# Kernel tuning notes

Hardware: AMD Instinct MI355X
Metric: run time of the kernel (lower is better)

Reference implementation:

```python
import jax, jax.numpy as jnp
import numpy as np

EPS = 1e-5
GROUPS = 32


def group_norm(x, gamma, beta):
    b, c, h, w = x.shape
    xg = x.reshape(b, GROUPS, c // GROUPS, h, w)
    mu = xg.mean(axis=(2, 3, 4), keepdims=True)
    var = xg.var(axis=(2, 3, 4), keepdims=True)
    xn = ((xg - mu) * jax.lax.rsqrt(var + EPS)).reshape(b, c, h, w)
    return xn * gamma[None, :, None, None] + beta[None, :, None, None]


def setup_inputs() -> dict:
    key = jax.random.key(0)
    ks = jax.random.split(key, 4)
    b, c, h, w = 4, 512, 64, 64
    x = jax.random.normal(ks[0], (b, c, h, w), dtype=jnp.float32)
    gn_w = jnp.ones((c,), jnp.float32)
    gn_b = jnp.zeros((c,), jnp.float32)
    qkv_w = jax.random.normal(ks[1], (3 * c, c), dtype=jnp.float32) * (c ** -0.5)
    qkv_b = jnp.zeros((3 * c,), jnp.float32)
    out_w = jax.random.normal(ks[2], (c, c), dtype=jnp.float32) * (c ** -0.5)
    out_b = jnp.zeros((c,), jnp.float32)
    return {"x": x, "gn_w": gn_w, "gn_b": gn_b, "qkv_w": qkv_w,
            "qkv_b": qkv_b, "out_w": out_w, "out_b": out_b}


def reference(x, gn_w, gn_b, qkv_w, qkv_b, out_w, out_b):
    b, c, hh, ww = x.shape
    n = hh * ww
    h = group_norm(x, gn_w, gn_b)
    # 1x1 conv == per-pixel matmul over channels
    qkv = jnp.einsum('bchw,oc->bohw', h, qkv_w) + qkv_b[None, :, None, None]
    q, k, v = jnp.split(qkv, 3, axis=1)
    q = q.transpose(0, 2, 3, 1).reshape(b, n, c)   # (b, n, c)
    k = k.reshape(b, c, n)                          # (b, c, n)
    v = v.transpose(0, 2, 3, 1).reshape(b, n, c)   # (b, n, c)
    attn = jax.nn.softmax(jnp.einsum('bnc,bcm->bnm', q, k) * (c ** -0.5), axis=-1)
    out = jnp.einsum('bnm,bmc->bnc', attn, v)
    out = out.reshape(b, hh, ww, c).transpose(0, 3, 1, 2)
    out = jnp.einsum('bchw,oc->bohw', out, out_w) + out_b[None, :, None, None]
    return out + x
```

## Files before the change

### kernel.cpp

```cpp
#include <hip/hip_runtime.h>
#include <cmath>

#define NB 4
#define NC 512
#define NN 4096
#define ATTN_SCALE 0.04419417382415922f

typedef __bf16 bf16x8 __attribute__((ext_vector_type(8)));
typedef float floatx4 __attribute__((ext_vector_type(4)));

__device__ __forceinline__ unsigned short f2bf(float f) {
    union { float f; unsigned int u; } v; v.f = f;
    return (unsigned short)((v.u + 0x7fffu + ((v.u >> 16) & 1u)) >> 16);
}
__device__ __forceinline__ unsigned short f2bf_trunc(float f) {
    union { float f; unsigned int u; } v; v.f = f;
    return (unsigned short)(v.u >> 16);
}
__device__ __forceinline__ float bf2f(unsigned short u) {
    union { unsigned int u; float f; } v; v.u = ((unsigned int)u) << 16;
    return v.f;
}

__device__ __forceinline__ void gload_lds16(const unsigned short* gp, unsigned short* lp) {
    __builtin_amdgcn_global_load_lds(
        (const __attribute__((address_space(1))) void*)gp,
        (__attribute__((address_space(3))) void*)lp, 16, 0, 0);
}

__global__ __launch_bounds__(256) void gn_partial_kernel(
    const float* __restrict__ x, float* __restrict__ part)
{
    int blk = blockIdx.x;
    int bg = blk >> 3, sub = blk & 7;
    const float4* xv = (const float4*)(x + (size_t)bg * 16 * NN + (size_t)sub * 8192);
    float s1 = 0.f, s2 = 0.f;
#pragma unroll
    for (int i = 0; i < 8; ++i) {
        float4 v = xv[threadIdx.x + i * 256];
        s1 += v.x + v.y + v.z + v.w;
        s2 += v.x * v.x + v.y * v.y + v.z * v.z + v.w * v.w;
    }
#pragma unroll
    for (int off = 32; off; off >>= 1) {
        s1 += __shfl_xor(s1, off, 64);
        s2 += __shfl_xor(s2, off, 64);
    }
    __shared__ float r1[4], r2[4];
    int lane = threadIdx.x & 63, w = threadIdx.x >> 6;
    if (lane == 0) { r1[w] = s1; r2[w] = s2; }
    __syncthreads();
    if (threadIdx.x == 0) {
        part[blk * 2]     = r1[0] + r1[1] + r1[2] + r1[3];
        part[blk * 2 + 1] = r2[0] + r2[1] + r2[2] + r2[3];
    }
}

__global__ __launch_bounds__(128) void gn_final_kernel(
    const float* __restrict__ part, const float* __restrict__ gw,
    const float* __restrict__ gb, float* __restrict__ ss)
{
    int tg = threadIdx.x;
    int b = tg >> 5, g = tg & 31;
    float s1 = 0.f, s2 = 0.f;
#pragma unroll
    for (int s = 0; s < 8; ++s) {
        s1 += part[(tg * 8 + s) * 2];
        s2 += part[(tg * 8 + s) * 2 + 1];
    }
    float mean = s1 * (1.0f / 65536.0f);
    float var  = s2 * (1.0f / 65536.0f) - mean * mean;
    float rstd = rsqrtf(var + 1e-5f);
#pragma unroll
    for (int i = 0; i < 16; ++i) {
        int c = g * 16 + i;
        float sc = rstd * gw[c];
        ss[b * NC + c] = sc;
        ss[2048 + b * NC + c] = gb[c] - mean * sc;
    }
}

__global__ __launch_bounds__(256) void wconv_kernel(
    const float* __restrict__ qkv_w, const float* __restrict__ out_w,
    unsigned short* __restrict__ wq, unsigned short* __restrict__ wo)
{
    int i = blockIdx.x * 256 + threadIdx.x;
    const int NQ = 1536 * 512;
    if (i < NQ) wq[i] = f2bf(qkv_w[i]);
    else        wo[i - NQ] = f2bf(out_w[i - NQ]);
}

__global__ __launch_bounds__(256) void htnorm_kernel(
    const float* __restrict__ x, const float* __restrict__ ss,
    unsigned short* __restrict__ ht)
{
    int b = blockIdx.z;
    int c0 = blockIdx.y * 32, n0 = blockIdx.x * 32;
    __shared__ float T[32][33];
    int tx = threadIdx.x & 31, ty = threadIdx.x >> 5;
    const float* xb = x + ((size_t)b * NC + c0) * NN;
    const float* sc = ss + b * NC + c0;
    const float* sh = ss + 2048 + b * NC + c0;
#pragma unroll
    for (int i = 0; i < 4; ++i) {
        int c = ty + i * 8;
        T[c][tx] = xb[(size_t)c * NN + n0 + tx] * sc[c] + sh[c];
    }
    __syncthreads();
    unsigned short* hb = ht + ((size_t)b * NN + n0) * NC + c0;
#pragma unroll
    for (int i = 0; i < 4; ++i) {
        int n = ty + i * 8;
        hb[(size_t)n * NC + tx] = f2bf(T[tx][n]);
    }
}

template<int MODE, int BM, int BN>
__global__ __launch_bounds__(256, 3) void mfma_gemm(
    const unsigned short* __restrict__ Abase,
    const unsigned short* __restrict__ Bbase,
    const float* __restrict__ e0, const float* __restrict__ e1,
    float* __restrict__ outf,
    unsigned short* __restrict__ ob0, unsigned short* __restrict__ ob1)
{
    constexpr int K = 512;
    constexpr int FI = BM / 32;
    constexpr int FJ = BN / 32;
    const int z = blockIdx.z;
    const size_t bnc = (size_t)NN * NC;
    const size_t bss = (size_t)NN * NN;

    const unsigned short* A;
    const unsigned short* B;
    if constexpr (MODE == 0)      { A = Abase + (size_t)z * bnc; B = Bbase; }
    else if constexpr (MODE == 1) { A = Abase; B = Bbase + (size_t)z * bnc; }
    else if constexpr (MODE == 2) { A = Abase + (size_t)z * bnc; B = Bbase + (size_t)z * bnc; }
    else                          { A = Abase; B = Bbase + (size_t)z * bnc; }

    const int m0 = blockIdx.y * BM;
    const int n0 = blockIdx.x * BN;

    __shared__ __attribute__((aligned(16))) unsigned short As[BM * 32];
    __shared__ __attribute__((aligned(16))) unsigned short Bs[BN * 32];

    const int t = threadIdx.x;
    const int lane = t & 63;
    const int w = t >> 6;
    const int wr = w >> 1, wc = w & 1;

    const int sr = w * 16 + (lane >> 2);
    const int sc8 = (lane & 3) * 8;
    const int lds_elem = w * 512;

    floatx4 acc[FI][FJ] = {};

    for (int k0 = 0; k0 < K; k0 += 32) {
#pragma unroll
        for (int s = 0; s < BM / 64; ++s)
            gload_lds16(A + (size_t)(m0 + s * 64 + sr) * K + k0 + sc8,
                        As + s * 2048 + lds_elem);
#pragma unroll
        for (int s = 0; s < BN / 64; ++s)
            gload_lds16(B + (size_t)(n0 + s * 64 + sr) * K + k0 + sc8,
                        Bs + s * 2048 + lds_elem);
        __syncthreads();

        bf16x8 af[FI], bfr[FJ];
        const unsigned short* Ab = As + ((wr * (BM / 2) + (lane & 15)) * 32) + (lane >> 4) * 8;
        const unsigned short* Bb = Bs + ((wc * (BN / 2) + (lane & 15)) * 32) + (lane >> 4) * 8;
#pragma unroll
        for (int i = 0; i < FI; ++i) af[i]  = *(const bf16x8*)(Ab + i * 16 * 32);
#pragma unroll
        for (int j = 0; j < FJ; ++j) bfr[j] = *(const bf16x8*)(Bb + j * 16 * 32);
#pragma unroll
        for (int i = 0; i < FI; ++i)
#pragma unroll
            for (int j = 0; j < FJ; ++j)
                acc[i][j] = __builtin_amdgcn_mfma_f32_16x16x32_bf16(
                    af[i], bfr[j], acc[i][j], 0, 0, 0);
        __syncthreads();
    }

    const int fr = lane >> 4;
    const int fc = lane & 15;

    if constexpr (MODE == 2) {
        float rs[FI][4];
#pragma unroll
        for (int i = 0; i < FI; ++i)
#pragma unroll
            for (int r = 0; r < 4; ++r) rs[i][r] = 0.f;
#pragma unroll
        for (int i = 0; i < FI; ++i) {
#pragma unroll
            for (int j = 0; j < FJ; ++j) {
                int n = n0 + wc * (BN / 2) + j * 16 + fc;
                int mbase = m0 + wr * (BM / 2) + i * 16 + fr * 4;
#pragma unroll
                for (int r = 0; r < 4; ++r) {
                    float e = __expf(acc[i][j][r]);
                    ob0[(size_t)z * bss + (size_t)(mbase + r) * NN + n] = f2bf_trunc(e);
                    rs[i][r] += e;
                }
            }
        }
#pragma unroll
        for (int i = 0; i < FI; ++i) {
#pragma unroll
            for (int r = 0; r < 4; ++r) {
                float v = rs[i][r];
                v += __shfl_xor(v, 1, 16);
                v += __shfl_xor(v, 2, 16);
                v += __shfl_xor(v, 4, 16);
                v += __shfl_xor(v, 8, 16);
                if (fc == 0) {
                    int m = m0 + wr * (BM / 2) + i * 16 + fr * 4 + r;
                    atomicAdd(&outf[z * NN + m], v);
                }
            }
        }
        return;
    }

#pragma unroll
    for (int i = 0; i < FI; ++i) {
#pragma unroll
        for (int j = 0; j < FJ; ++j) {
            int n = n0 + wc * (BN / 2) + j * 16 + fc;
            int mbase = m0 + wr * (BM / 2) + i * 16 + fr * 4;
#pragma unroll
            for (int r = 0; r < 4; ++r) {
                int m = mbase + r;
                float val = acc[i][j][r];
                if constexpr (MODE == 0) {
                    val += e0[n];
                    if (n < 512) ob0[((size_t)z * NN + m) * NC + n] = f2bf(val * ATTN_SCALE);
                    else         ob1[((size_t)z * NN + m) * NC + (n - 512)] = f2bf(val);
                } else if constexpr (MODE == 1) {
                    val += e0[1024 + m];
                    ob0[((size_t)z * NC + m) * NN + n] = f2bf(val);
                } else {
                    size_t idx = ((size_t)z * NC + m) * NN + n;
                    outf[idx] = val + e0[m] + e1[idx];
                }
            }
        }
    }
}

__global__ __launch_bounds__(256, 4) void pv_gemm(
    const unsigned short* __restrict__ Abase,
    const unsigned short* __restrict__ Bbase,
    const float* __restrict__ L,
    unsigned short* __restrict__ Ob)
{
    const int id = blockIdx.x;
    const int xcd = id & 7;
    const int j0 = id >> 3;
    const int ct = j0 & 3;
    const int pairl = j0 >> 2;
    const int p = pairl * 8 + xcd;
    const int ptile = p & 63, z = p >> 6;

    const size_t bss = (size_t)NN * NN, bnc = (size_t)NN * NC;
    const unsigned short* A = Abase + (size_t)z * bss;
    const unsigned short* B = Bbase + (size_t)z * bnc;
    const int m0 = ptile * 64;
    const int n0 = ct * 128;

    __shared__ __attribute__((aligned(16))) unsigned short As[64 * 64];
    __shared__ __attribute__((aligned(16))) unsigned short Bs[128 * 64];

    const int t = threadIdx.x;
    const int lane = t & 63;
    const int w = t >> 6;
    const int wr = w >> 1, wc = w & 1;

    const int sr = w * 8 + (lane >> 3);
    const int scs = ((lane & 7) ^ (lane >> 3)) * 8;
    const int lds_elem = w * 512;

    floatx4 acc[2][4] = {};

    for (int k0 = 0; k0 < NN; k0 += 64) {
#pragma unroll
        for (int s = 0; s < 2; ++s)
            gload_lds16(A + (size_t)(m0 + s * 32 + sr) * NN + k0 + scs,
                        As + s * 2048 + lds_elem);
#pragma unroll
        for (int s = 0; s < 4; ++s)
            gload_lds16(B + (size_t)(n0 + s * 32 + sr) * NN + k0 + scs,
                        Bs + s * 2048 + lds_elem);
        __syncthreads();

        bf16x8 af[2][2], bfr[4][2];
#pragma unroll
        for (int i = 0; i < 2; ++i) {
            const int ra = wr * 32 + i * 16 + (lane & 15);
#pragma unroll
            for (int kk = 0; kk < 2; ++kk)
                af[i][kk] = *(const bf16x8*)(As + ra * 64 +
                    (((kk * 4 + (lane >> 4)) ^ (ra & 7)) * 8));
        }
#pragma unroll
        for (int jj = 0; jj < 4; ++jj) {
            const int rb = wc * 64 + jj * 16 + (lane & 15);
#pragma unroll
            for (int kk = 0; kk < 2; ++kk)
                bfr[jj][kk] = *(const bf16x8*)(Bs + rb * 64 +
                    (((kk * 4 + (lane >> 4)) ^ (rb & 7)) * 8));
        }
#pragma unroll
        for (int kk = 0; kk < 2; ++kk)
#pragma unroll
            for (int i = 0; i < 2; ++i)
#pragma unroll
                for (int jj = 0; jj < 4; ++jj)
                    acc[i][jj] = __builtin_amdgcn_mfma_f32_16x16x32_bf16(
                        af[i][kk], bfr[jj][kk], acc[i][jj], 0, 0, 0);
        __syncthreads();
    }

    const int fr = lane >> 4;
    const int fc = lane & 15;
#pragma unroll
    for (int i = 0; i < 2; ++i) {
#pragma unroll
        for (int r = 0; r < 4; ++r) {
            int m = m0 + wr * 32 + i * 16 + fr * 4 + r;
            float linv = 1.0f / L[z * NN + m];
#pragma unroll
            for (int jj = 0; jj < 4; ++jj) {
                int n = n0 + wc * 64 + jj * 16 + fc;
                Ob[(size_t)z * bnc + (size_t)m * NC + n] = f2bf(acc[i][jj][r] * linv);
            }
        }
    }
}

extern "C" void kernel_launch(void* const* d_in, const int* in_sizes, int n_in,
                              void* d_out, int out_size, void* d_ws, size_t ws_size,
                              hipStream_t stream)
{
    const float* x     = (const float*)d_in[0];
    const float* gn_w  = (const float*)d_in[1];
    const float* gn_b  = (const float*)d_in[2];
    const float* qkv_w = (const float*)d_in[3];
    const float* qkv_b = (const float*)d_in[4];
    const float* out_w = (const float*)d_in[5];
    const float* out_b = (const float*)d_in[6];
    float* out = (float*)d_out;

    const size_t bnc = (size_t)NN * NC;
    char* w = (char*)d_ws;
    float* ss   = (float*)w;                 w += 16384;
    float* part = (float*)w;                 w += 8192;
    float* Lsum = (float*)w;                 w += (size_t)NB * NN * 4;
    unsigned short* wq = (unsigned short*)w; w += (size_t)1536 * 512 * 2;
    unsigned short* wo = (unsigned short*)w; w += (size_t)512 * 512 * 2;
    unsigned short* qt = (unsigned short*)w; w += NB * bnc * 2;
    unsigned short* kt = (unsigned short*)w; w += NB * bnc * 2;
    unsigned short* vt = (unsigned short*)w; w += NB * bnc * 2;
    unsigned short* SP = (unsigned short*)w; w += (size_t)NB * NN * NN * 2;
    unsigned short* ht = SP;
    unsigned short* Ob = qt;

    hipMemsetAsync(Lsum, 0, (size_t)NB * NN * sizeof(float), stream);

    gn_partial_kernel<<<1024, 256, 0, stream>>>(x, part);
    gn_final_kernel<<<1, 128, 0, stream>>>(part, gn_w, gn_b, ss);
    wconv_kernel<<<(1536 * 512 + 512 * 512) / 256, 256, 0, stream>>>(qkv_w, out_w, wq, wo);
    htnorm_kernel<<<dim3(NN / 32, NC / 32, NB), 256, 0, stream>>>(x, ss, ht);

    mfma_gemm<0, 128, 128><<<dim3(1024 / 128, NN / 128, NB), 256, 0, stream>>>(
        ht, wq, qkv_b, nullptr, nullptr, qt, kt);
    mfma_gemm<1, 128, 128><<<dim3(NN / 128, 512 / 128, NB), 256, 0, stream>>>(
        wq + (size_t)1024 * 512, ht, qkv_b, nullptr, nullptr, vt, nullptr);

    mfma_gemm<2, 128, 128><<<dim3(NN / 128, NN / 128, NB), 256, 0, stream>>>(
        qt, kt, nullptr, nullptr, Lsum, SP, nullptr);
    pv_gemm<<<dim3(1024), 256, 0, stream>>>(SP, vt, Lsum, Ob);

    mfma_gemm<4, 128, 128><<<dim3(NN / 128, 512 / 128, NB), 256, 0, stream>>>(
        wo, Ob, out_b, x, out, nullptr, nullptr);
}
```

Before: 378.2 us.

## Double-buffer LDS in MFMA GEMM, swizzle LDS layout, retile skinny GEMMs

Makes the GEMM's shared-memory staging double-buffered, so the global-to-LDS loads for the next K slice are issued before the MFMAs on the current slice run. It also applies an XOR swizzle to the K-slot column of the LDS tiles to cut bank conflicts on the fragment reads. The V projection and output projection GEMMs switch to 64x128 tiles with a higher minimum-blocks launch bound, giving more blocks on those small grids. In exchange the kernel uses twice the LDS, and the explicit vmcnt waits may limit how much load latency is actually hidden.

Measured after the change: 377.6 us. Within noise of the previous version (-0.1%).

```diff
diff --git a/kernel.cpp b/kernel.cpp
--- a/kernel.cpp
+++ b/kernel.cpp
@@ -115,8 +115,8 @@
     }
 }
 
-template<int MODE, int BM, int BN>
-__global__ __launch_bounds__(256, 3) void mfma_gemm(
+template<int MODE, int BM, int BN, int MINB>
+__global__ __launch_bounds__(256, MINB) void mfma_gemm(
     const unsigned short* __restrict__ Abase,
     const unsigned short* __restrict__ Bbase,
     const float* __restrict__ e0, const float* __restrict__ e1,
@@ -124,6 +124,7 @@
     unsigned short* __restrict__ ob0, unsigned short* __restrict__ ob1)
 {
     constexpr int K = 512;
+    constexpr int NT = K / 32;
     constexpr int FI = BM / 32;
     constexpr int FJ = BN / 32;
     const int z = blockIdx.z;
@@ -140,8 +141,8 @@
     const int m0 = blockIdx.y * BM;
     const int n0 = blockIdx.x * BN;
 
-    __shared__ __attribute__((aligned(16))) unsigned short As[BM * 32];
-    __shared__ __attribute__((aligned(16))) unsigned short Bs[BN * 32];
+    __shared__ __attribute__((aligned(16))) unsigned short As[2][BM * 32];
+    __shared__ __attribute__((aligned(16))) unsigned short Bs[2][BN * 32];
 
     const int t = threadIdx.x;
     const int lane = t & 63;
@@ -149,37 +150,55 @@
     const int wr = w >> 1, wc = w & 1;
 
     const int sr = w * 16 + (lane >> 2);
-    const int sc8 = (lane & 3) * 8;
+    const int scs = ((lane & 3) ^ ((lane >> 3) & 3)) * 8;
     const int lds_elem = w * 512;
+    const int kslot = lane >> 4;
 
     floatx4 acc[FI][FJ] = {};
 
-    for (int k0 = 0; k0 < K; k0 += 32) {
+    auto stage = [&](int buf, int k0) {
 #pragma unroll
         for (int s = 0; s < BM / 64; ++s)
-            gload_lds16(A + (size_t)(m0 + s * 64 + sr) * K + k0 + sc8,
-                        As + s * 2048 + lds_elem);
+            gload_lds16(A + (size_t)(m0 + s * 64 + sr) * K + k0 + scs,
+                        &As[buf][s * 2048 + lds_elem]);
 #pragma unroll
         for (int s = 0; s < BN / 64; ++s)
-            gload_lds16(B + (size_t)(n0 + s * 64 + sr) * K + k0 + sc8,
-                        Bs + s * 2048 + lds_elem);
-        __syncthreads();
-
+            gload_lds16(B + (size_t)(n0 + s * 64 + sr) * K + k0 + scs,
+                        &Bs[buf][s * 2048 + lds_elem]);
+    };
+
+    auto compute = [&](int buf) {
         bf16x8 af[FI], bfr[FJ];
-        const unsigned short* Ab = As + ((wr * (BM / 2) + (lane & 15)) * 32) + (lane >> 4) * 8;
-        const unsigned short* Bb = Bs + ((wc * (BN / 2) + (lane & 15)) * 32) + (lane >> 4) * 8;
-#pragma unroll
-        for (int i = 0; i < FI; ++i) af[i]  = *(const bf16x8*)(Ab + i * 16 * 32);
-#pragma unroll
-        for (int j = 0; j < FJ; ++j) bfr[j] = *(const bf16x8*)(Bb + j * 16 * 32);
+#pragma unroll
+        for (int i = 0; i < FI; ++i) {
+            const int ra = wr * (BM / 2) + i * 16 + (lane & 15);
+            af[i] = *(const bf16x8*)(&As[buf][ra * 32 + ((kslot ^ ((ra >> 1) & 3)) * 8)]);
+        }
+#pragma unroll
+        for (int j = 0; j < FJ; ++j) {
+            const int rb = wc * (BN / 2) + j * 16 + (lane & 15);
+            bfr[j] = *(const bf16x8*)(&Bs[buf][rb * 32 + ((kslot ^ ((rb >> 1) & 3)) * 8)]);
+        }
 #pragma unroll
         for (int i = 0; i < FI; ++i)
 #pragma unroll
             for (int j = 0; j < FJ; ++j)
                 acc[i][j] = __builtin_amdgcn_mfma_f32_16x16x32_bf16(
                     af[i], bfr[j], acc[i][j], 0, 0, 0);
+    };
+
+    stage(0, 0);
+    asm volatile("s_waitcnt vmcnt(0)" ::: "memory");
+    __syncthreads();
+    int cur = 0;
+    for (int kt = 0; kt < NT - 1; ++kt) {
+        stage(cur ^ 1, (kt + 1) * 32);
+        compute(cur);
+        asm volatile("s_waitcnt vmcnt(0)" ::: "memory");
         __syncthreads();
-    }
+        cur ^= 1;
+    }
+    compute(cur);
 
     const int fr = lane >> 4;
     const int fc = lane & 15;
@@ -372,15 +391,15 @@
     wconv_kernel<<<(1536 * 512 + 512 * 512) / 256, 256, 0, stream>>>(qkv_w, out_w, wq, wo);
     htnorm_kernel<<<dim3(NN / 32, NC / 32, NB), 256, 0, stream>>>(x, ss, ht);
 
-    mfma_gemm<0, 128, 128><<<dim3(1024 / 128, NN / 128, NB), 256, 0, stream>>>(
+    mfma_gemm<0, 128, 128, 3><<<dim3(1024 / 128, NN / 128, NB), 256, 0, stream>>>(
         ht, wq, qkv_b, nullptr, nullptr, qt, kt);
-    mfma_gemm<1, 128, 128><<<dim3(NN / 128, 512 / 128, NB), 256, 0, stream>>>(
+    mfma_gemm<1, 64, 128, 4><<<dim3(NN / 128, 512 / 64, NB), 256, 0, stream>>>(
         wq + (size_t)1024 * 512, ht, qkv_b, nullptr, nullptr, vt, nullptr);
 
-    mfma_gemm<2, 128, 128><<<dim3(NN / 128, NN / 128, NB), 256, 0, stream>>>(
+    mfma_gemm<2, 128, 128, 3><<<dim3(NN / 128, NN / 128, NB), 256, 0, stream>>>(
         qt, kt, nullptr, nullptr, Lsum, SP, nullptr);
     pv_gemm<<<dim3(1024), 256, 0, stream>>>(SP, vt, Lsum, Ob);
 
-    mfma_gemm<4, 128, 128><<<dim3(NN / 128, 512 / 128, NB), 256, 0, stream>>>(
+    mfma_gemm<4, 64, 128, 4><<<dim3(NN / 128, 512 / 64, NB), 256, 0, stream>>>(
         wo, Ob, out_b, x, out, nullptr, nullptr);
 }
```
